# Kernel tuning notes

Measured on AMD Instinct MI355X. Metric: run time of the kernel, lower is better.

Reference implementation:

```python
import jax, jax.numpy as jnp
import numpy as np

T_MIN, T_MAX = 0.03, 0.34
STEPS = 32
K_MAX = 2
N_DIMS = 2  # homology dimensions [0, 1]

B, C, H, W = 128, 64, 64, 64
P = 128  # persistence pairs per (b, c)


def setup_inputs() -> dict:
    key = jax.random.key(0)
    k1, k2, k3, k4 = jax.random.split(key, 4)
    x = jax.random.uniform(k1, (B, C, H, W), dtype=jnp.float32)
    birth_idx = jax.random.randint(k2, (B, C, P), 0, H * W)
    death_idx = jax.random.randint(k3, (B, C, P), 0, H * W)
    pair_dim = jax.random.randint(k4, (B, C, P), 0, N_DIMS)
    return {"x": x, "birth_idx": birth_idx, "death_idx": death_idx, "pair_dim": pair_dim}


def reference(x, birth_idx, death_idx, pair_dim):
    # x: [B, C, H, W]; indices: [B, C, P] into flattened H*W grid.
    tseq = jnp.linspace(T_MIN, T_MAX, STEPS).astype(x.dtype)  # [T]
    b_, c_, h_, w_ = x.shape
    xf = x.reshape(b_, c_, h_ * w_)
    births = jnp.take_along_axis(xf, birth_idx, axis=-1)  # [B, C, P]
    deaths = jnp.take_along_axis(xf, death_idx, axis=-1)  # [B, C, P]
    # Landscape triangle functions: max(min(t - birth, death - t), 0) -> [B, C, P, T]
    tri = jnp.maximum(jnp.minimum(tseq - births[..., None], deaths[..., None] - tseq), 0.0)
    # Mask pairs by their homology dimension -> [B, C, D, P, T]
    dims = jnp.arange(N_DIMS)
    mask = pair_dim[:, :, None, :, None] == dims[None, None, :, None, None]
    land = jnp.where(mask, tri[:, :, None, :, :], 0.0)
    # Top-K_max landscapes over pairs, per (dim, t): original does -sort(-land)[:K]
    land_t = jnp.swapaxes(land, -1, -2)  # [B, C, D, T, P]
    top, _ = jax.lax.top_k(land_t, K_MAX)  # [B, C, D, T, K]
    return jnp.swapaxes(top, -1, -2)  # [B, C, D, K, T]
```

## Files before the change

kernel.cpp:

```cpp
#include <hip/hip_runtime.h>


constexpr int P = 128;
constexpr float T_MIN = 0.03f;
constexpr float T_MAX = 0.34f;
constexpr float BIG = 1e30f;

__global__ __launch_bounds__(256) void pl_topk_kernel(
    const float* __restrict__ x,
    const int* __restrict__ birth_idx,
    const int* __restrict__ death_idx,
    const int* __restrict__ pair_dim,
    float* __restrict__ out)
{
    __shared__ float2 tab[4][2][130];

    const int lane = threadIdx.x & 63;
    const int w = threadIdx.x >> 6;
    const int wid = blockIdx.x * 4 + w;

    const int d_lane = lane >> 5;
    const int t_idx = lane & 31;
    const float t = T_MIN + (T_MAX - T_MIN) * (float)t_idx * (1.0f / 31.0f);

    const long pbase = (long)wid * P;
    const int2 bi = *reinterpret_cast<const int2*>(&birth_idx[pbase + 2 * lane]);
    const int2 di = *reinterpret_cast<const int2*>(&death_idx[pbase + 2 * lane]);
    const int2 dm = *reinterpret_cast<const int2*>(&pair_dim[pbase + 2 * lane]);

    const long xbase = (long)wid * 4096;
    const float xb0 = x[xbase + bi.x];
    const float xb1 = x[xbase + bi.y];
    const float xd0 = x[xbase + di.x];
    const float xd1 = x[xbase + di.y];

    const unsigned long long below = (lane == 63) ? ~0ull >> 1
                                                  : (1ull << lane) - 1ull;
    const unsigned long long a_d1 = __ballot(dm.x == 1);
    const unsigned long long b_d1 = __ballot(dm.y == 1);
    const unsigned long long a_d0 = ~a_d1;
    const unsigned long long b_d0 = ~b_d1;

    const int nA0 = __popcll(a_d0);
    const int nA1 = 64 - nA0;
    const int n0 = nA0 + __popcll(b_d0);
    const int n1 = P - n0;

    const unsigned long long myA = dm.x ? a_d1 : a_d0;
    const int posA = __popcll(myA & below);
    const unsigned long long myB = dm.y ? b_d1 : b_d0;
    const int posB = (dm.y ? nA1 : nA0) + __popcll(myB & below);

    tab[w][dm.x][posA] = make_float2(xb0, xd0);
    tab[w][dm.y][posB] = make_float2(xb1, xd1);
    if (lane == 0) tab[w][0][n0] = make_float2(BIG, -BIG);
    if (lane == 1) tab[w][1][n1] = make_float2(BIG, -BIG);

    asm volatile("s_waitcnt lgkmcnt(0)" ::: "memory");

    const int n_mine = d_lane ? n1 : n0;
    float m1 = 0.0f, m2 = 0.0f;
    const float2* tp = &tab[w][d_lane][0];
    #pragma unroll 2
    for (int p = 0; p < n_mine; p += 2) {
        const float4 e = *reinterpret_cast<const float4*>(&tp[p]);
        const float v0 = fminf(t - e.x, e.y - t);
        const float v1 = fminf(t - e.z, e.w - t);
        m2 = fmaxf(m2, fminf(m1, v0));
        m1 = fmaxf(m1, v0);
        m2 = fmaxf(m2, fminf(m1, v1));
        m1 = fmaxf(m1, v1);
    }

    float* o = out + (long)wid * 128;
    o[d_lane * 64 + t_idx] = m1;
    o[d_lane * 64 + 32 + t_idx] = m2;
}

extern "C" void kernel_launch(void* const* d_in, const int* in_sizes, int n_in,
                              void* d_out, int out_size, void* d_ws, size_t ws_size,
                              hipStream_t stream) {
    const float* x = (const float*)d_in[0];
    const int* birth_idx = (const int*)d_in[1];
    const int* death_idx = (const int*)d_in[2];
    const int* pair_dim = (const int*)d_in[3];
    float* out = (float*)d_out;

    dim3 grid(2048), block(256);
    hipLaunchKernelGGL(pl_topk_kernel, grid, block, 0, stream,
                       x, birth_idx, death_idx, pair_dim, out);
}
```

Measured before the change: 26.14 us.

## Stage full per-channel x slice in LDS and gather births/deaths from shared memory

Each wave now loads its whole 4096-float x slice with coalesced float4 loads into LDS, then gathers birth/death values from LDS instead of issuing four random global loads per lane. The same LDS region is reused as the compact pair table. This reads the full 16KB slice per wave instead of about 512 scattered floats, trading more global bandwidth and 64KB of LDS per block (lower occupancy) for coalesced access. Reusing the slice buffer for the table depends on same-wave ordering via lgkmcnt waits.

After: 28.34 us. +8.4%, slower.

```diff
diff --git a/kernel.cpp b/kernel.cpp
--- a/kernel.cpp
+++ b/kernel.cpp
@@ -13,7 +13,7 @@
     const int* __restrict__ pair_dim,
     float* __restrict__ out)
 {
-    __shared__ float2 tab[4][2][130];
+    __shared__ float slice[4][4096];
 
     const int lane = threadIdx.x & 63;
     const int w = threadIdx.x >> 6;
@@ -28,39 +28,46 @@
     const int2 di = *reinterpret_cast<const int2*>(&death_idx[pbase + 2 * lane]);
     const int2 dm = *reinterpret_cast<const int2*>(&pair_dim[pbase + 2 * lane]);
 
-    const long xbase = (long)wid * 4096;
-    const float xb0 = x[xbase + bi.x];
-    const float xb1 = x[xbase + bi.y];
-    const float xd0 = x[xbase + di.x];
-    const float xd1 = x[xbase + di.y];
+    const float4* xs = reinterpret_cast<const float4*>(x + (long)wid * 4096);
+    float4 s[16];
+    #pragma unroll
+    for (int c = 0; c < 16; ++c) s[c] = xs[c * 64 + lane];
 
-    const unsigned long long below = (lane == 63) ? ~0ull >> 1
-                                                  : (1ull << lane) - 1ull;
-    const unsigned long long a_d1 = __ballot(dm.x == 1);
-    const unsigned long long b_d1 = __ballot(dm.y == 1);
-    const unsigned long long a_d0 = ~a_d1;
-    const unsigned long long b_d0 = ~b_d1;
+    const unsigned long long below = (1ull << lane) - 1ull;
+    const unsigned long long a1 = __ballot(dm.x == 1);
+    const unsigned long long b1 = __ballot(dm.y == 1);
+    const int nA0 = __popcll(~a1);
+    const int nA1 = 64 - nA0;
+    const int n0 = nA0 + __popcll(~b1);
+    const int n1 = P - n0;
+    const int posA = __popcll((dm.x ? a1 : ~a1) & below);
+    const int posB = (dm.y ? nA1 : nA0) + __popcll((dm.y ? b1 : ~b1) & below);
 
-    const int nA0 = __popcll(a_d0);
-    const int nA1 = 64 - nA0;
-    const int n0 = nA0 + __popcll(b_d0);
-    const int n1 = P - n0;
+    float* sl = slice[w];
+    #pragma unroll
+    for (int c = 0; c < 16; ++c)
+        *reinterpret_cast<float4*>(&sl[(c * 64 + lane) * 4]) = s[c];
 
-    const unsigned long long myA = dm.x ? a_d1 : a_d0;
-    const int posA = __popcll(myA & below);
-    const unsigned long long myB = dm.y ? b_d1 : b_d0;
-    const int posB = (dm.y ? nA1 : nA0) + __popcll(myB & below);
+    asm volatile("s_waitcnt lgkmcnt(0)" ::: "memory");
 
-    tab[w][dm.x][posA] = make_float2(xb0, xd0);
-    tab[w][dm.y][posB] = make_float2(xb1, xd1);
-    if (lane == 0) tab[w][0][n0] = make_float2(BIG, -BIG);
-    if (lane == 1) tab[w][1][n1] = make_float2(BIG, -BIG);
+    const float xb0 = sl[bi.x];
+    const float xb1 = sl[bi.y];
+    const float xd0 = sl[di.x];
+    const float xd1 = sl[di.y];
+
+    asm volatile("s_waitcnt lgkmcnt(0)" ::: "memory");
+
+    float2* tab = reinterpret_cast<float2*>(sl);
+    tab[dm.x * 130 + posA] = make_float2(xb0, xd0);
+    tab[dm.y * 130 + posB] = make_float2(xb1, xd1);
+    if (lane == 0) tab[n0] = make_float2(BIG, -BIG);
+    if (lane == 1) tab[130 + n1] = make_float2(BIG, -BIG);
 
     asm volatile("s_waitcnt lgkmcnt(0)" ::: "memory");
 
     const int n_mine = d_lane ? n1 : n0;
     float m1 = 0.0f, m2 = 0.0f;
-    const float2* tp = &tab[w][d_lane][0];
+    const float2* tp = &tab[d_lane * 130];
     #pragma unroll 2
     for (int p = 0; p < n_mine; p += 2) {
         const float4 e = *reinterpret_cast<const float4*>(&tp[p]);
```
